# Optimization experiments

Measured on AMD Instinct MI355X. Metric: run time of the kernel, lower is better.

The kernel has to match this reference:

```python
import jax, jax.numpy as jnp
import numpy as np
from jax import lax

D, H, HD, DEPTH = 200, 10, 20, 12   # embed_dim, heads, head_dim, depth
NCH, A = 64, 8                       # EEG channels x time windows -> 512 patches (+cls)
NUM_REL = (2 * NCH - 1) * (2 * A - 1) + 3  # 1908


def make_rel_index(wh, ww):
    # exact port of the torch relative_position_index construction
    coords = np.stack(np.meshgrid(np.arange(wh), np.arange(ww), indexing='ij')).reshape(2, -1)
    rel = (coords[:, :, None] - coords[:, None, :]).transpose(1, 2, 0)
    rel[..., 0] += wh - 1
    rel[..., 1] += ww - 1
    rel[..., 0] *= 2 * ww - 1
    n = wh * ww + 1
    num_rel = (2 * wh - 1) * (2 * ww - 1) + 3
    idx = np.zeros((n, n), dtype=np.int32)
    idx[1:, 1:] = rel.sum(-1)
    idx[0, :] = num_rel - 3
    idx[:, 0] = num_rel - 2
    idx[0, 0] = num_rel - 1
    return idx


def gelu(x):
    return jax.nn.gelu(x, approximate=False)


def layer_norm(x, g, b, eps=1e-6):
    m = x.mean(-1, keepdims=True)
    v = ((x - m) ** 2).mean(-1, keepdims=True)
    return (x - m) * lax.rsqrt(v + eps) * g + b


def group_norm(x, g, b, groups=4, eps=1e-5):
    B, C, Hh, W = x.shape
    xr = x.reshape(B, groups, C // groups, Hh, W)
    m = xr.mean((2, 3, 4), keepdims=True)
    v = ((xr - m) ** 2).mean((2, 3, 4), keepdims=True)
    xr = ((xr - m) * lax.rsqrt(v + eps)).reshape(B, C, Hh, W)
    return xr * g[None, :, None, None] + b[None, :, None, None]


def conv2d(x, w, b, stride, pad):
    y = lax.conv_general_dilated(x, w, window_strides=stride, padding=pad,
                                 dimension_numbers=('NCHW', 'OIHW', 'NCHW'))
    return y + b[None, :, None, None]


def setup_inputs() -> dict:
    B = 8
    key = jax.random.key(0)
    ks = iter(jax.random.split(key, 40))
    rn = lambda shape, s=0.02: jax.random.normal(next(ks), shape, dtype=jnp.float32) * s
    z = lambda shape: jnp.zeros(shape, jnp.float32)
    o = lambda shape: jnp.ones(shape, jnp.float32)
    inp = {}
    inp['x'] = jax.random.normal(next(ks), (B, NCH, A, 200), dtype=jnp.float32)
    inp['conv1_w'] = rn((8, 1, 1, 15), 0.1); inp['conv1_b'] = z(8)
    inp['gn1_g'] = o(8); inp['gn1_b'] = z(8)
    inp['conv2_w'] = rn((8, 8, 1, 3), 0.1); inp['conv2_b'] = z(8)
    inp['gn2_g'] = o(8); inp['gn2_b'] = z(8)
    inp['conv3_w'] = rn((8, 8, 1, 3), 0.1); inp['conv3_b'] = z(8)
    inp['gn3_g'] = o(8); inp['gn3_b'] = z(8)
    inp['cls_token'] = rn((1, 1, D)); inp['pos_embed'] = rn((1, NCH + 1, D))
    inp['time_embed'] = rn((1, 16, D))
    inp['ln1_g'] = o((DEPTH, D)); inp['ln1_b'] = z((DEPTH, D))
    inp['qkv_w'] = rn((DEPTH, 3 * D, D))
    inp['rel_bias_table'] = rn((DEPTH, NUM_REL, H))
    inp['proj_w'] = rn((DEPTH, D, D)); inp['proj_b'] = z((DEPTH, D))
    inp['gamma1'] = 0.1 * o((DEPTH, D))
    inp['ln2_g'] = o((DEPTH, D)); inp['ln2_b'] = z((DEPTH, D))
    inp['fc1_w'] = rn((DEPTH, 4 * D, D)); inp['fc1_b'] = z((DEPTH, 4 * D))
    inp['fc2_w'] = rn((DEPTH, D, 4 * D)); inp['fc2_b'] = z((DEPTH, D))
    inp['gamma2'] = 0.1 * o((DEPTH, D))
    inp['fc_norm_g'] = o(D); inp['fc_norm_b'] = z(D)
    inp['head_w'] = rn((4, D)); inp['head_b'] = z(4)
    inp['rel_pos_index'] = jnp.asarray(make_rel_index(NCH, A))
    return inp


def reference(x, conv1_w, conv1_b, gn1_g, gn1_b, conv2_w, conv2_b, gn2_g, gn2_b,
              conv3_w, conv3_b, gn3_g, gn3_b, cls_token, pos_embed, time_embed,
              ln1_g, ln1_b, qkv_w, rel_bias_table, proj_w, proj_b, gamma1,
              ln2_g, ln2_b, fc1_w, fc1_b, fc2_w, fc2_b, gamma2,
              fc_norm_g, fc_norm_b, head_w, head_b, rel_pos_index):
    B = x.shape[0]
    # TemporalConv patch embed: (B, NCH, A, 200) -> (B, NCH*A, D)
    h = x.reshape(B, 1, NCH * A, -1)
    h = gelu(group_norm(conv2d(h, conv1_w, conv1_b, (1, 8), [(0, 0), (7, 7)]), gn1_g, gn1_b))
    h = gelu(group_norm(conv2d(h, conv2_w, conv2_b, (1, 1), [(0, 0), (1, 1)]), gn2_g, gn2_b))
    h = gelu(group_norm(conv2d(h, conv3_w, conv3_b, (1, 1), [(0, 0), (1, 1)]), gn3_g, gn3_b))
    h = h.transpose(0, 2, 3, 1).reshape(B, NCH * A, D)  # 'B C NA T -> B NA (T C)'
    # cls token + per-electrode pos embed + temporal embed
    h = jnp.concatenate([jnp.broadcast_to(cls_token, (B, 1, D)), h], axis=1)
    pos_p = jnp.repeat(pos_embed[:, 1:, None, :], A, axis=2).reshape(1, NCH * A, D)
    h = h + jnp.concatenate([pos_embed[:, :1], pos_p], axis=1)
    te = jnp.broadcast_to(time_embed[:, None, :A, :], (1, NCH, A, D)).reshape(1, NCH * A, D)
    h = jnp.concatenate([h[:, :1], h[:, 1:] + te], axis=1)
    N = h.shape[1]  # 513
    scale = HD ** -0.5
    for d in range(DEPTH):
        y = layer_norm(h, ln1_g[d], ln1_b[d])
        qkv = (y @ qkv_w[d].T).reshape(B, N, 3, H, HD).transpose(2, 0, 3, 1, 4)
        q, k, v = qkv[0], qkv[1], qkv[2]
        attn = jnp.einsum('bhnd,bhmd->bhnm', q * scale, k)
        attn = attn + rel_bias_table[d][rel_pos_index].transpose(2, 0, 1)[None]
        attn = jax.nn.softmax(attn, axis=-1)
        o = jnp.einsum('bhnm,bhmd->bhnd', attn, v)
        o = o.transpose(0, 2, 1, 3).reshape(B, N, D) @ proj_w[d].T + proj_b[d]
        h = h + gamma1[d] * o
        y = layer_norm(h, ln2_g[d], ln2_b[d])
        y = gelu(y @ fc1_w[d].T + fc1_b[d]) @ fc2_w[d].T + fc2_b[d]
        h = h + gamma2[d] * y
    pooled = layer_norm(h[:, 1:].mean(1), fc_norm_g, fc_norm_b)  # use_mean_pooling
    return pooled @ head_w.T + head_b
```

## Files before the change

### kernel.cpp

```cpp
#include <hip/hip_runtime.h>
#include <math.h>

#define DEV static __device__ __forceinline__

typedef __attribute__((ext_vector_type(8))) short bf16x8;
typedef __attribute__((ext_vector_type(4))) float f32x4;

DEV float gelu_exact(float x) {
    return 0.5f * x * (1.0f + erff(x * 0.70710678118654752f));
}

DEV short f2bf(float f) {
    union { float f; unsigned u; } v; v.f = f;
    unsigned r = v.u + 0x7FFF + ((v.u >> 16) & 1);
    return (short)(r >> 16);
}

DEV float bf2f(unsigned short b) {
    union { unsigned u; float f; } v; v.u = ((unsigned)b) << 16;
    return v.f;
}

DEV unsigned pack2bf(float a, float b) {
    return ((unsigned)(unsigned short)f2bf(a)) | (((unsigned)(unsigned short)f2bf(b)) << 16);
}

DEV void gload_lds16(const void* g, void* lds) {
    __builtin_amdgcn_global_load_lds(
        (const __attribute__((address_space(1))) void*)g,
        (__attribute__((address_space(3))) void*)lds, 16, 0, 0);
}

__global__ void conv1_kernel(const float* __restrict__ x, const float* __restrict__ w,
                             const float* __restrict__ bias, float* __restrict__ out) {
    int idx = blockIdx.x * blockDim.x + threadIdx.x;
    const int total = 8 * 8 * 512 * 25;
    if (idx >= total) return;
    int ow = idx % 25;
    int p  = (idx / 25) % 512;
    int oc = (idx / (25 * 512)) % 8;
    int b  = idx / (25 * 512 * 8);
    const float* xp = x + b * 512 * 200 + p * 200;
    const float* wp = w + oc * 15;
    float acc = bias[oc];
    int t0 = ow * 8 - 7;
#pragma unroll
    for (int k = 0; k < 15; k++) {
        int t = t0 + k;
        if (t >= 0 && t < 200) acc += wp[k] * xp[t];
    }
    out[idx] = acc;
}

__global__ void conv3x1_kernel(const float* __restrict__ in, const float* __restrict__ w,
                               const float* __restrict__ bias, float* __restrict__ out) {
    int idx = blockIdx.x * blockDim.x + threadIdx.x;
    const int total = 8 * 8 * 512 * 25;
    if (idx >= total) return;
    int ow = idx % 25;
    int p  = (idx / 25) % 512;
    int oc = (idx / 12800) & 7;
    int b  = idx / 102400;
    float acc = bias[oc];
#pragma unroll
    for (int ic = 0; ic < 8; ic++) {
        const float* ip = in + b * 102400 + ic * 12800 + p * 25;
        const float* wp = w + oc * 24 + ic * 3;
        if (ow > 0)  acc += wp[0] * ip[ow - 1];
        acc += wp[1] * ip[ow];
        if (ow < 24) acc += wp[2] * ip[ow + 1];
    }
    out[idx] = acc;
}

__global__ void gn_stats_kernel(const float* __restrict__ buf, float* __restrict__ stats) {
    int b = blockIdx.x >> 2, g = blockIdx.x & 3;
    const float* base = buf + b * 102400 + g * 2 * 12800;
    float s = 0.f, s2 = 0.f;
    for (int l = threadIdx.x; l < 25600; l += 256) {
        float v = base[l];
        s += v; s2 += v * v;
    }
    __shared__ float ss[256], ss2[256];
    ss[threadIdx.x] = s; ss2[threadIdx.x] = s2;
    __syncthreads();
    for (int o = 128; o; o >>= 1) {
        if (threadIdx.x < o) { ss[threadIdx.x] += ss[threadIdx.x + o]; ss2[threadIdx.x] += ss2[threadIdx.x + o]; }
        __syncthreads();
    }
    if (threadIdx.x == 0) {
        float m = ss[0] / 25600.f;
        float v = ss2[0] / 25600.f - m * m;
        stats[blockIdx.x * 2] = m;
        stats[blockIdx.x * 2 + 1] = v;
    }
}

__global__ void gn_apply_kernel(float* __restrict__ buf, const float* __restrict__ stats,
                                const float* __restrict__ g, const float* __restrict__ bb) {
    int idx = blockIdx.x * blockDim.x + threadIdx.x;
    if (idx >= 8 * 102400) return;
    int c = (idx / 12800) & 7;
    int b = idx / 102400;
    int grp = c >> 1;
    float m = stats[(b * 4 + grp) * 2];
    float v = stats[(b * 4 + grp) * 2 + 1];
    float val = (buf[idx] - m) * rsqrtf(v + 1e-5f) * g[c] + bb[c];
    buf[idx] = gelu_exact(val);
}

__global__ void embed_kernel(const float* __restrict__ conv, const float* __restrict__ cls,
                             const float* __restrict__ pos, const float* __restrict__ te,
                             float* __restrict__ h) {
    int idx = blockIdx.x * blockDim.x + threadIdx.x;
    if (idx >= 8 * 513 * 200) return;
    int d = idx % 200;
    int n = (idx / 200) % 513;
    int b = idx / (200 * 513);
    float val;
    if (n == 0) {
        val = cls[d] + pos[d];
    } else {
        int p = n - 1;
        int t = d >> 3;
        int c = d & 7;
        val = conv[b * 102400 + c * 12800 + p * 25 + t];
        int ch = p >> 3, tw = p & 7;
        val += pos[(1 + ch) * 200 + d] + te[tw * 200 + d];
    }
    h[idx] = val;
}

__global__ void convpad_kernel(const float* __restrict__ src, short* __restrict__ dst,
                               int R, int K, int KP) {
    int idx = blockIdx.x * blockDim.x + threadIdx.x;
    int total = R * (KP >> 2);
    if (idx >= total) return;
    int r = idx / (KP >> 2);
    int c4 = (idx - r * (KP >> 2)) << 2;
    short4 o;
    if (c4 + 3 < K) {
        float4 f = *(const float4*)&src[(size_t)r * K + c4];
        o.x = f2bf(f.x); o.y = f2bf(f.y); o.z = f2bf(f.z); o.w = f2bf(f.w);
    } else {
        o.x = (c4 + 0 < K) ? f2bf(src[(size_t)r * K + c4 + 0]) : (short)0;
        o.y = (c4 + 1 < K) ? f2bf(src[(size_t)r * K + c4 + 1]) : (short)0;
        o.z = (c4 + 2 < K) ? f2bf(src[(size_t)r * K + c4 + 2]) : (short)0;
        o.w = (c4 + 3 < K) ? f2bf(src[(size_t)r * K + c4 + 3]) : (short)0;
    }
    *(short4*)&dst[(size_t)r * KP + c4] = o;
}

__global__ __launch_bounds__(256) void bias_lds_kernel(const float* __restrict__ table,
                                                       const int* __restrict__ ridx,
                                                       short* __restrict__ bias) {
    __shared__ float tl[1908];
    const int qt = blockIdx.x, hh = blockIdx.y, d = blockIdx.z;
    const float* tab = table + d * 19080;
    for (int i = threadIdx.x; i < 1908; i += 256) tl[i] = tab[i * 10 + hh];
    __syncthreads();
    const int q0 = qt * 32;
    const int nrows = min(32, 513 - q0);
    short* obase = bias + ((size_t)d * 10 + hh) * 513 * 576;
#pragma unroll 2
    for (int lin = threadIdx.x; lin < nrows * 144; lin += 256) {
        int r = lin / 144, j = lin % 144;
        int q = q0 + r;
        const int* rp = ridx + q * 513;
        int k0 = j * 4;
        float v[4];
#pragma unroll
        for (int e = 0; e < 4; e++) {
            int k = k0 + e;
            v[e] = (k < 513) ? tl[rp[k]] : 0.f;
        }
        uint2 pk;
        pk.x = pack2bf(v[0], v[1]);
        pk.y = pack2bf(v[2], v[3]);
        *(uint2*)&obase[(size_t)q * 576 + k0] = pk;
    }
}

__global__ __launch_bounds__(256) void ln_kernel(const float* __restrict__ in,
                                                 const float* __restrict__ g,
                                                 const float* __restrict__ b,
                                                 short* __restrict__ out) {
    int row = blockIdx.x * 4 + (threadIdx.x >> 6);
    int lane = threadIdx.x & 63;
    const float* x = in + (size_t)row * 200;
    float v[4];
    float s = 0.f;
#pragma unroll
    for (int i = 0; i < 4; i++) {
        int d = lane + i * 64;
        v[i] = (d < 200) ? x[d] : 0.f;
        s += v[i];
    }
#pragma unroll
    for (int o = 32; o; o >>= 1) s += __shfl_xor(s, o);
    float mean = s * (1.f / 200.f);
    float s2 = 0.f;
#pragma unroll
    for (int i = 0; i < 4; i++) {
        int d = lane + i * 64;
        float dv = (d < 200) ? (v[i] - mean) : 0.f;
        s2 += dv * dv;
    }
#pragma unroll
    for (int o = 32; o; o >>= 1) s2 += __shfl_xor(s2, o);
    float rstd = rsqrtf(s2 * (1.f / 200.f) + 1e-6f);
#pragma unroll
    for (int i = 0; i < 4; i++) {
        int d = lane + i * 64;
        float val = (d < 200) ? (v[i] - mean) * rstd * g[d] + b[d] : 0.f;
        out[(size_t)row * 256 + d] = f2bf(val);
    }
}

template <int EPI, int BM, int BN>
__global__ __launch_bounds__(256) void gemm_bf(const short* __restrict__ A,
                                               const short* __restrict__ W,
                                               float* __restrict__ Cf,
                                               short* __restrict__ Cb,
                                               const float* __restrict__ res,
                                               const float* __restrict__ bias,
                                               const float* __restrict__ gamma,
                                               int M, int N, int KP, int ldc, int NPout,
                                               short* __restrict__ Qb = nullptr,
                                               short* __restrict__ Kb = nullptr,
                                               short* __restrict__ Vt = nullptr) {
    constexpr int WM = BM / 2, WN = BN / 2;
    constexpr int AM = WM / 16, BNr = WN / 16;
    constexpr int LOADS = (BM + BN) / 32;
    __shared__ __align__(16) short Ss[2][(BM + BN) * 64];

    const int tid = threadIdx.x;
    const int w = tid >> 6, l = tid & 63;
    const int wm = (w >> 1) * WM, wn = (w & 1) * WN;
    const int bm = blockIdx.y * BM, bn = blockIdx.x * BN;

    f32x4 acc[AM][BNr] = {};

    auto stage = [&](int buf, int k0) {
#pragma unroll
        for (int it = 0; it < LOADS; it++) {
            int lin = it * 256 + tid;
            int row = lin >> 3, slot = lin & 7;
            int srcslot = slot ^ (row & 7);
            const short* g;
            if (it * 32 < BM) {
                g = A + (size_t)(bm + row) * KP + k0 + srcslot * 8;
            } else {
                g = W + (size_t)(bn + row - BM) * KP + k0 + srcslot * 8;
            }
            gload_lds16(g, (char*)Ss[buf] + lin * 16);
        }
    };

    const int nk = KP >> 6;
    stage(0, 0);
    int cur = 0;
    for (int kstep = 0; kstep < nk; kstep++) {
        if (kstep + 1 < nk) {
            stage(cur ^ 1, (kstep + 1) << 6);
            if constexpr (LOADS == 6)      asm volatile("s_waitcnt vmcnt(6)" ::: "memory");
            else if constexpr (LOADS == 4) asm volatile("s_waitcnt vmcnt(4)" ::: "memory");
            else                           asm volatile("s_waitcnt vmcnt(3)" ::: "memory");
        } else {
            asm volatile("s_waitcnt vmcnt(0)" ::: "memory");
        }
        __builtin_amdgcn_s_barrier();

        const char* Sc = (const char*)Ss[cur];
#pragma unroll
        for (int kk = 0; kk < 2; kk++) {
            const int kbyte = kk * 64 + (l >> 4) * 16;
            bf16x8 af[AM], bfr[BNr];
#pragma unroll
            for (int i = 0; i < AM; i++) {
                int r = wm + i * 16 + (l & 15);
                af[i] = *(const bf16x8*)(Sc + r * 128 + (kbyte ^ ((r & 7) << 4)));
            }
#pragma unroll
            for (int j = 0; j < BNr; j++) {
                int r = BM + wn + j * 16 + (l & 15);
                bfr[j] = *(const bf16x8*)(Sc + r * 128 + (kbyte ^ ((r & 7) << 4)));
            }
#pragma unroll
            for (int i = 0; i < AM; i++)
#pragma unroll
                for (int j = 0; j < BNr; j++)
                    acc[i][j] = __builtin_amdgcn_mfma_f32_16x16x32_bf16(af[i], bfr[j], acc[i][j], 0, 0, 0);
        }
        __builtin_amdgcn_s_barrier();
        cur ^= 1;
    }

    const int col0 = bn + wn + (l & 15);
    const int rbase = (l >> 4) * 4;
#pragma unroll
    for (int i = 0; i < AM; i++) {
#pragma unroll
        for (int r = 0; r < 4; r++) {
            int gm = bm + wm + i * 16 + rbase + r;
            if (gm >= M) continue;
#pragma unroll
            for (int j = 0; j < BNr; j++) {
                int gn = col0 + j * 16;
                float v = acc[i][j][r];
                if (EPI == 1) {
                    if (gn < N) Cf[(size_t)gm * ldc + gn] =
                        res[(size_t)gm * ldc + gn] + gamma[gn] * (v + bias[gn]);
                } else if (EPI == 2) {
                    if (gn < NPout)
                        Cb[(size_t)gm * ldc + gn] = (gn < N) ? f2bf(gelu_exact(v + bias[gn])) : (short)0;
                } else {
                    if (gn < 600) {
                        int bb2 = gm / 513, n = gm - bb2 * 513;
                        if (gn < 200) {
                            int hq = gn / 20, dq = gn - hq * 20;
                            Qb[((size_t)(bb2 * 10 + hq) * 576 + n) * 32 + dq] =
                                f2bf(v * 0.22360679774997896f);
                        } else if (gn < 400) {
                            int gk = gn - 200, hk = gk / 20, dk = gk - hk * 20;
                            Kb[((size_t)(bb2 * 10 + hk) * 576 + n) * 32 + dk] = f2bf(v);
                        } else {
                            int gv = gn - 400, hv = gv / 20, dv2 = gv - hv * 20;
                            Vt[((size_t)(bb2 * 10 + hv) * 32 + dv2) * 576 + n] = f2bf(v);
                        }
                    }
                }
            }
        }
    }
}

__global__ __launch_bounds__(256) void attn_mfma2(const short* __restrict__ Qb,
                                                  const short* __restrict__ Kb,
                                                  const short* __restrict__ Vt,
                                                  const short* __restrict__ biasb,
                                                  short* __restrict__ ob) {
    __shared__ __align__(16) short Klds[2][64 * 32];
    __shared__ __align__(16) short Vlds[2][32 * 64];
    __shared__ __align__(16) short Pl[4 * 16 * 72];

    const int orig = blockIdx.x;
    const int wg = (orig & 7) * 90 + (orig >> 3);
    const int hh = wg / 72;
    const int rem = wg % 72;
    const int qt = rem >> 3, b = rem & 7;

    const int t = threadIdx.x, wave = t >> 6, l = t & 63;
    const int lq = l & 15, hi = l >> 4;
    const int n = qt * 64 + wave * 16 + lq;
    const int nc = min(n, 512);

    const size_t bh = (size_t)(b * 10 + hh);
    const short* Kbase = Kb + bh * 576 * 32;
    const short* Vbase = Vt + bh * 32 * 576;
    const short* Brow  = biasb + ((size_t)hh * 513 + nc) * 576;

    bf16x8 qf = *(const bf16x8*)&Qb[(bh * 576 + nc) * 32 + hi * 8];

    const int krow = t >> 2, kch = t & 3;
    const short* ksrc = Kbase + (size_t)krow * 32 + (kch ^ ((krow >> 2) & 3)) * 8;
    const int vrow = t >> 3, vch = t & 7;
    const short* vsrc = Vbase + (size_t)vrow * 576 + (vch ^ (vrow & 7)) * 8;

    float mrun = -1e30f, lsum = 0.f;
    f32x4 oacc0 = {}, oacc1 = {};
    const f32x4 zero4 = {};

    gload_lds16(ksrc, (char*)Klds[0] + t * 16);
    gload_lds16(vsrc, (char*)Vlds[0] + t * 16);

    int cur = 0;
    for (int kt = 0; kt < 9; kt++) {
        const int koff = kt * 64;

        uint2 bl[4];
#pragma unroll
        for (int c = 0; c < 4; c++)
            bl[c] = *(const uint2*)&Brow[koff + c * 16 + hi * 4];

        if (kt < 8) {
            const int knext = koff + 64;
            gload_lds16(ksrc + (size_t)knext * 32, (char*)Klds[cur ^ 1] + t * 16);
            gload_lds16(vsrc + knext, (char*)Vlds[cur ^ 1] + t * 16);
            asm volatile("s_waitcnt vmcnt(2)" ::: "memory");
        } else {
            asm volatile("s_waitcnt vmcnt(0)" ::: "memory");
        }
        __builtin_amdgcn_s_barrier();

        const short* Kc = Klds[cur];
        const short* Vc = Vlds[cur];

        f32x4 s[4];
        __builtin_amdgcn_s_setprio(1);
#pragma unroll
        for (int c = 0; c < 4; c++) {
            int r = c * 16 + lq;
            bf16x8 kf = *(const bf16x8*)((const char*)Kc + r * 64 + ((hi ^ ((lq >> 2) & 3)) << 4));
            s[c] = __builtin_amdgcn_mfma_f32_16x16x32_bf16(kf, qf, zero4, 0, 0, 0);
        }
        __builtin_amdgcn_s_setprio(0);

        float sv[4][4];
        float tm = -1e30f;
#pragma unroll
        for (int c = 0; c < 4; c++) {
            float bv[4] = { bf2f((unsigned short)(bl[c].x & 0xFFFF)), bf2f((unsigned short)(bl[c].x >> 16)),
                            bf2f((unsigned short)(bl[c].y & 0xFFFF)), bf2f((unsigned short)(bl[c].y >> 16)) };
            int kglob = koff + c * 16 + hi * 4;
#pragma unroll
            for (int r = 0; r < 4; r++) {
                float val = s[c][r] + bv[r];
                if (kglob + r > 512) val = -1e30f;
                sv[c][r] = val;
                tm = fmaxf(tm, val);
            }
        }
        tm = fmaxf(tm, __shfl_xor(tm, 16));
        tm = fmaxf(tm, __shfl_xor(tm, 32));
        float mnew = fmaxf(mrun, tm);
        float resc = __expf(mrun - mnew);
        mrun = mnew;

        float ts = 0.f;
#pragma unroll
        for (int c = 0; c < 4; c++) {
            float p0 = __expf(sv[c][0] - mnew);
            float p1 = __expf(sv[c][1] - mnew);
            float p2 = __expf(sv[c][2] - mnew);
            float p3 = __expf(sv[c][3] - mnew);
            ts += (p0 + p1) + (p2 + p3);
            uint2 pk;
            pk.x = pack2bf(p0, p1);
            pk.y = pack2bf(p2, p3);
            *(uint2*)&Pl[wave * 1152 + lq * 72 + c * 16 + hi * 4] = pk;
        }
        ts += __shfl_xor(ts, 16);
        ts += __shfl_xor(ts, 32);
        lsum = lsum * resc + ts;
        oacc0 *= resc;
        oacc1 *= resc;

        __builtin_amdgcn_s_setprio(1);
#pragma unroll
        for (int kc = 0; kc < 2; kc++) {
            bf16x8 pf = *(const bf16x8*)&Pl[wave * 1152 + lq * 72 + kc * 32 + hi * 8];
            bf16x8 vf0 = *(const bf16x8*)((const char*)Vc + lq * 128 +
                                          (((kc * 4 + hi) ^ (lq & 7)) << 4));
            bf16x8 vf1 = *(const bf16x8*)((const char*)Vc + (16 + lq) * 128 +
                                          (((kc * 4 + hi) ^ (lq & 7)) << 4));
            oacc0 = __builtin_amdgcn_mfma_f32_16x16x32_bf16(vf0, pf, oacc0, 0, 0, 0);
            oacc1 = __builtin_amdgcn_mfma_f32_16x16x32_bf16(vf1, pf, oacc1, 0, 0, 0);
        }
        __builtin_amdgcn_s_setprio(0);

        __builtin_amdgcn_s_barrier();
        cur ^= 1;
    }

    if (n < 513) {
        float inv = 1.f / lsum;
        short* op = ob + (size_t)(b * 513 + n) * 256 + hh * 20;
        {
            uint2 pk;
            pk.x = pack2bf(oacc0[0] * inv, oacc0[1] * inv);
            pk.y = pack2bf(oacc0[2] * inv, oacc0[3] * inv);
            *(uint2*)&op[hi * 4] = pk;
        }
        if (hi == 0) {
            uint2 pk;
            pk.x = pack2bf(oacc1[0] * inv, oacc1[1] * inv);
            pk.y = pack2bf(oacc1[2] * inv, oacc1[3] * inv);
            *(uint2*)&op[16] = pk;
        }
    }
}

__global__ __launch_bounds__(256) void final_kernel(const float* __restrict__ h,
                                                    const float* __restrict__ g,
                                                    const float* __restrict__ bb,
                                                    const float* __restrict__ hw,
                                                    const float* __restrict__ hb,
                                                    float* __restrict__ out) {
    __shared__ float pool[256];
    __shared__ float red[256];
    int b = blockIdx.x, t = threadIdx.x;
    float s = 0.f;
    if (t < 200) {
        const float* hp = h + b * 513 * 200 + 200 + t;
        for (int p = 0; p < 512; p++) s += hp[p * 200];
        s *= (1.f / 512.f);
    }
    pool[t] = (t < 200) ? s : 0.f;
    red[t] = pool[t];
    __syncthreads();
    for (int o = 128; o; o >>= 1) {
        if (t < o) red[t] += red[t + o];
        __syncthreads();
    }
    float mean = red[0] / 200.f;
    __syncthreads();
    float dv = (t < 200) ? (pool[t] - mean) : 0.f;
    red[t] = dv * dv;
    __syncthreads();
    for (int o = 128; o; o >>= 1) {
        if (t < o) red[t] += red[t + o];
        __syncthreads();
    }
    float var = red[0] / 200.f;
    float rstd = rsqrtf(var + 1e-6f);
    __syncthreads();
    if (t < 200) pool[t] = (pool[t] - mean) * rstd * g[t] + bb[t];
    __syncthreads();
    if (t < 4) {
        float acc = hb[t];
        for (int d2 = 0; d2 < 200; d2++) acc += pool[d2] * hw[t * 200 + d2];
        out[b * 4 + t] = acc;
    }
}

extern "C" void kernel_launch(void* const* d_in, const int* in_sizes, int n_in,
                              void* d_out, int out_size, void* d_ws, size_t ws_size,
                              hipStream_t stream) {
    const float* x        = (const float*)d_in[0];
    const float* conv1_w  = (const float*)d_in[1];
    const float* conv1_b  = (const float*)d_in[2];
    const float* gn1_g    = (const float*)d_in[3];
    const float* gn1_b    = (const float*)d_in[4];
    const float* conv2_w  = (const float*)d_in[5];
    const float* conv2_b  = (const float*)d_in[6];
    const float* gn2_g    = (const float*)d_in[7];
    const float* gn2_b    = (const float*)d_in[8];
    const float* conv3_w  = (const float*)d_in[9];
    const float* conv3_b  = (const float*)d_in[10];
    const float* gn3_g    = (const float*)d_in[11];
    const float* gn3_b    = (const float*)d_in[12];
    const float* cls_tok  = (const float*)d_in[13];
    const float* pos_emb  = (const float*)d_in[14];
    const float* time_emb = (const float*)d_in[15];
    const float* ln1_g    = (const float*)d_in[16];
    const float* ln1_b    = (const float*)d_in[17];
    const float* qkv_w    = (const float*)d_in[18];
    const float* rel_tab  = (const float*)d_in[19];
    const float* proj_w   = (const float*)d_in[20];
    const float* proj_b   = (const float*)d_in[21];
    const float* gamma1   = (const float*)d_in[22];
    const float* ln2_g    = (const float*)d_in[23];
    const float* ln2_b    = (const float*)d_in[24];
    const float* fc1_w    = (const float*)d_in[25];
    const float* fc1_b    = (const float*)d_in[26];
    const float* fc2_w    = (const float*)d_in[27];
    const float* fc2_b    = (const float*)d_in[28];
    const float* gamma2   = (const float*)d_in[29];
    const float* fcn_g    = (const float*)d_in[30];
    const float* fcn_b    = (const float*)d_in[31];
    const float* head_w   = (const float*)d_in[32];
    const float* head_b   = (const float*)d_in[33];
    const int*   rel_idx  = (const int*)d_in[34];

    char* p = (char*)d_ws;
    float* h    = (float*)p; p += 3283200;
    char* qreg = p;
    float* c1   = (float*)qreg;
    float* c2   = c1 + 819200;
    short* Qb   = (short*)qreg;
    short* Kb   = Qb + 1474560;
    short* Vt   = Kb + 1474560;
    short* mlp  = (short*)qreg;
    p += 9849600;
    short* y    = (short*)p; p += 2101248;
    short* ob   = (short*)p; p += 2101248;
    short* wqkv = (short*)p; p += 3686400;
    short* wproj= (short*)p; p += 1228800;
    short* wfc1 = (short*)p; p += 4915200;
    short* wfc2 = (short*)p; p += 3993600;
    short* biasb= (short*)p; p += 12 * 5909760;
    float* stats= (float*)p;

    convpad_kernel<<<(7200 * 64 + 255) / 256, 256, 0, stream>>>(qkv_w, wqkv, 7200, 200, 256);
    convpad_kernel<<<(2400 * 64 + 255) / 256, 256, 0, stream>>>(proj_w, wproj, 2400, 200, 256);
    convpad_kernel<<<(9600 * 64 + 255) / 256, 256, 0, stream>>>(fc1_w, wfc1, 9600, 200, 256);
    convpad_kernel<<<(2400 * 208 + 255) / 256, 256, 0, stream>>>(fc2_w, wfc2, 2400, 800, 832);
    bias_lds_kernel<<<dim3(17, 10, 12), 256, 0, stream>>>(rel_tab, rel_idx, biasb);
    hipMemsetAsync(ob, 0, 2101248, stream);

    conv1_kernel<<<3200, 256, 0, stream>>>(x, conv1_w, conv1_b, c1);
    gn_stats_kernel<<<32, 256, 0, stream>>>(c1, stats);
    gn_apply_kernel<<<3200, 256, 0, stream>>>(c1, stats, gn1_g, gn1_b);
    conv3x1_kernel<<<3200, 256, 0, stream>>>(c1, conv2_w, conv2_b, c2);
    gn_stats_kernel<<<32, 256, 0, stream>>>(c2, stats);
    gn_apply_kernel<<<3200, 256, 0, stream>>>(c2, stats, gn2_g, gn2_b);
    conv3x1_kernel<<<3200, 256, 0, stream>>>(c2, conv3_w, conv3_b, c1);
    gn_stats_kernel<<<32, 256, 0, stream>>>(c1, stats);
    gn_apply_kernel<<<3200, 256, 0, stream>>>(c1, stats, gn3_g, gn3_b);
    embed_kernel<<<(820800 + 255) / 256, 256, 0, stream>>>(c1, cls_tok, pos_emb, time_emb, h);

    hipMemsetAsync(Qb, 0, 3 * 1474560 * 2, stream);

    for (int d = 0; d < 12; d++) {
        ln_kernel<<<1026, 256, 0, stream>>>(h, ln1_g + d * 200, ln1_b + d * 200, y);
        gemm_bf<3, 32, 64><<<dim3(10, 129), 256, 0, stream>>>(y, wqkv + d * 153600,
                                                              nullptr, nullptr, nullptr, nullptr, nullptr,
                                                              4104, 600, 256, 0, 0, Qb, Kb, Vt);
        attn_mfma2<<<720, 256, 0, stream>>>(Qb, Kb, Vt, biasb + (size_t)d * 2954880, ob);
        gemm_bf<1, 32, 64><<<dim3(4, 129), 256, 0, stream>>>(ob, wproj + d * 51200, h, nullptr,
                                                             h, proj_b + d * 200, gamma1 + d * 200,
                                                             4104, 200, 256, 200, 0);
        ln_kernel<<<1026, 256, 0, stream>>>(h, ln2_g + d * 200, ln2_b + d * 200, y);
        gemm_bf<2, 32, 64><<<dim3(13, 129), 256, 0, stream>>>(y, wfc1 + d * 204800, nullptr, mlp,
                                                              nullptr, fc1_b + d * 800, nullptr,
                                                              4104, 800, 256, 832, 832);
        gemm_bf<1, 32, 64><<<dim3(4, 129), 256, 0, stream>>>(mlp, wfc2 + d * 166400, h, nullptr,
                                                             h, fc2_b + d * 200, gamma2 + d * 200,
                                                             4104, 200, 832, 200, 0);
    }

    final_kernel<<<8, 256, 0, stream>>>(h, fcn_g, fcn_b, head_w, head_b, (float*)d_out);
}
```

Baseline: 982.2 us.

## Deepen attention K/V pipeline to four LDS buffers and split GroupNorm stats

The attention kernel now cycles through four LDS buffers for K and V and prefetches two tiles ahead. It drops the trailing barrier in each iteration and loads the next tile's bias values one step early into registers. The goal is to hide global-load latency and barrier cost in the key loop, at the price of more LDS per block and a vmcnt wait scheme that must be counted exactly. Separately, GroupNorm statistics move from 32 blocks to 512 blocks that write partial sums, which a small second kernel combines, so that more of the GPU works on this step.

```diff
diff --git a/kernel.cpp b/kernel.cpp
--- a/kernel.cpp
+++ b/kernel.cpp
@@ -73,27 +73,43 @@
     out[idx] = acc;
 }
 
-__global__ void gn_stats_kernel(const float* __restrict__ buf, float* __restrict__ stats) {
-    int b = blockIdx.x >> 2, g = blockIdx.x & 3;
-    const float* base = buf + b * 102400 + g * 2 * 12800;
+__global__ __launch_bounds__(256) void gn_stats1(const float* __restrict__ buf,
+                                                 float* __restrict__ part) {
+    int bg = blockIdx.x >> 4, ch = blockIdx.x & 15;
+    const float* base = buf + (bg >> 2) * 102400 + (bg & 3) * 25600 + ch * 1600;
     float s = 0.f, s2 = 0.f;
-    for (int l = threadIdx.x; l < 25600; l += 256) {
-        float v = base[l];
-        s += v; s2 += v * v;
-    }
-    __shared__ float ss[256], ss2[256];
-    ss[threadIdx.x] = s; ss2[threadIdx.x] = s2;
+    int t4 = threadIdx.x * 4;
+#pragma unroll
+    for (int off = 0; off < 1600; off += 1024) {
+        int l = t4 + off;
+        if (l < 1600) {
+            float4 v = *(const float4*)&base[l];
+            s  += v.x + v.y + v.z + v.w;
+            s2 += v.x * v.x + v.y * v.y + v.z * v.z + v.w * v.w;
+        }
+    }
+#pragma unroll
+    for (int o = 32; o; o >>= 1) { s += __shfl_xor(s, o); s2 += __shfl_xor(s2, o); }
+    __shared__ float red[4][2];
+    if ((threadIdx.x & 63) == 0) { red[threadIdx.x >> 6][0] = s; red[threadIdx.x >> 6][1] = s2; }
     __syncthreads();
-    for (int o = 128; o; o >>= 1) {
-        if (threadIdx.x < o) { ss[threadIdx.x] += ss[threadIdx.x + o]; ss2[threadIdx.x] += ss2[threadIdx.x + o]; }
-        __syncthreads();
-    }
     if (threadIdx.x == 0) {
-        float m = ss[0] / 25600.f;
-        float v = ss2[0] / 25600.f - m * m;
-        stats[blockIdx.x * 2] = m;
-        stats[blockIdx.x * 2 + 1] = v;
-    }
+        part[blockIdx.x * 2]     = red[0][0] + red[1][0] + red[2][0] + red[3][0];
+        part[blockIdx.x * 2 + 1] = red[0][1] + red[1][1] + red[2][1] + red[3][1];
+    }
+}
+
+__global__ void gn_stats2(const float* __restrict__ part, float* __restrict__ stats) {
+    int i = threadIdx.x;
+    if (i >= 32) return;
+    float s = 0.f, q = 0.f;
+    for (int c = 0; c < 16; c++) {
+        s += part[(i * 16 + c) * 2];
+        q += part[(i * 16 + c) * 2 + 1];
+    }
+    float m = s / 25600.f;
+    stats[i * 2] = m;
+    stats[i * 2 + 1] = q / 25600.f - m * m;
 }
 
 __global__ void gn_apply_kernel(float* __restrict__ buf, const float* __restrict__ stats,
@@ -335,13 +351,13 @@
     }
 }
 
-__global__ __launch_bounds__(256) void attn_mfma2(const short* __restrict__ Qb,
+__global__ __launch_bounds__(256) void attn_mfma3(const short* __restrict__ Qb,
                                                   const short* __restrict__ Kb,
                                                   const short* __restrict__ Vt,
                                                   const short* __restrict__ biasb,
                                                   short* __restrict__ ob) {
-    __shared__ __align__(16) short Klds[2][64 * 32];
-    __shared__ __align__(16) short Vlds[2][32 * 64];
+    __shared__ __align__(16) short Klds[4][64 * 32];
+    __shared__ __align__(16) short Vlds[4][32 * 64];
     __shared__ __align__(16) short Pl[4 * 16 * 72];
 
     const int orig = blockIdx.x;
@@ -371,30 +387,37 @@
     f32x4 oacc0 = {}, oacc1 = {};
     const f32x4 zero4 = {};
 
+    uint2 bl_cur[4], bl_next[4];
+#pragma unroll
+    for (int c = 0; c < 4; c++)
+        bl_cur[c] = *(const uint2*)&Brow[c * 16 + hi * 4];
     gload_lds16(ksrc, (char*)Klds[0] + t * 16);
     gload_lds16(vsrc, (char*)Vlds[0] + t * 16);
-
-    int cur = 0;
+    gload_lds16(ksrc + 64 * 32, (char*)Klds[1] + t * 16);
+    gload_lds16(vsrc + 64, (char*)Vlds[1] + t * 16);
+
     for (int kt = 0; kt < 9; kt++) {
         const int koff = kt * 64;
 
-        uint2 bl[4];
-#pragma unroll
-        for (int c = 0; c < 4; c++)
-            bl[c] = *(const uint2*)&Brow[koff + c * 16 + hi * 4];
-
         if (kt < 8) {
-            const int knext = koff + 64;
-            gload_lds16(ksrc + (size_t)knext * 32, (char*)Klds[cur ^ 1] + t * 16);
-            gload_lds16(vsrc + knext, (char*)Vlds[cur ^ 1] + t * 16);
-            asm volatile("s_waitcnt vmcnt(2)" ::: "memory");
+#pragma unroll
+            for (int c = 0; c < 4; c++)
+                bl_next[c] = *(const uint2*)&Brow[koff + 64 + c * 16 + hi * 4];
+        }
+        if (kt < 7) {
+            const int knext = koff + 128;
+            gload_lds16(ksrc + (size_t)knext * 32, (char*)Klds[(kt + 2) & 3] + t * 16);
+            gload_lds16(vsrc + knext, (char*)Vlds[(kt + 2) & 3] + t * 16);
+            asm volatile("s_waitcnt vmcnt(8)" ::: "memory");
+        } else if (kt == 7) {
+            asm volatile("s_waitcnt vmcnt(6)" ::: "memory");
         } else {
             asm volatile("s_waitcnt vmcnt(0)" ::: "memory");
         }
         __builtin_amdgcn_s_barrier();
 
-        const short* Kc = Klds[cur];
-        const short* Vc = Vlds[cur];
+        const short* Kc = Klds[kt & 3];
+        const short* Vc = Vlds[kt & 3];
 
         f32x4 s[4];
         __builtin_amdgcn_s_setprio(1);
@@ -410,8 +433,8 @@
         float tm = -1e30f;
 #pragma unroll
         for (int c = 0; c < 4; c++) {
-            float bv[4] = { bf2f((unsigned short)(bl[c].x & 0xFFFF)), bf2f((unsigned short)(bl[c].x >> 16)),
-                            bf2f((unsigned short)(bl[c].y & 0xFFFF)), bf2f((unsigned short)(bl[c].y >> 16)) };
+            float bv[4] = { bf2f((unsigned short)(bl_cur[c].x & 0xFFFF)), bf2f((unsigned short)(bl_cur[c].x >> 16)),
+                            bf2f((unsigned short)(bl_cur[c].y & 0xFFFF)), bf2f((unsigned short)(bl_cur[c].y >> 16)) };
             int kglob = koff + c * 16 + hi * 4;
 #pragma unroll
             for (int r = 0; r < 4; r++) {
@@ -459,8 +482,8 @@
         }
         __builtin_amdgcn_s_setprio(0);
 
-        __builtin_amdgcn_s_barrier();
-        cur ^= 1;
+#pragma unroll
+        for (int c = 0; c < 4; c++) bl_cur[c] = bl_next[c];
     }
 
     if (n < 513) {
@@ -580,7 +603,8 @@
     short* wfc1 = (short*)p; p += 4915200;
     short* wfc2 = (short*)p; p += 3993600;
     short* biasb= (short*)p; p += 12 * 5909760;
-    float* stats= (float*)p;
+    float* stats= (float*)p; p += 256;
+    float* part = (float*)p;
 
     convpad_kernel<<<(7200 * 64 + 255) / 256, 256, 0, stream>>>(qkv_w, wqkv, 7200, 200, 256);
     convpad_kernel<<<(2400 * 64 + 255) / 256, 256, 0, stream>>>(proj_w, wproj, 2400, 200, 256);
@@ -590,13 +614,16 @@
     hipMemsetAsync(ob, 0, 2101248, stream);
 
     conv1_kernel<<<3200, 256, 0, stream>>>(x, conv1_w, conv1_b, c1);
-    gn_stats_kernel<<<32, 256, 0, stream>>>(c1, stats);
+    gn_stats1<<<512, 256, 0, stream>>>(c1, part);
+    gn_stats2<<<1, 64, 0, stream>>>(part, stats);
     gn_apply_kernel<<<3200, 256, 0, stream>>>(c1, stats, gn1_g, gn1_b);
     conv3x1_kernel<<<3200, 256, 0, stream>>>(c1, conv2_w, conv2_b, c2);
-    gn_stats_kernel<<<32, 256, 0, stream>>>(c2, stats);
+    gn_stats1<<<512, 256, 0, stream>>>(c2, part);
+    gn_stats2<<<1, 64, 0, stream>>>(part, stats);
     gn_apply_kernel<<<3200, 256, 0, stream>>>(c2, stats, gn2_g, gn2_b);
     conv3x1_kernel<<<3200, 256, 0, stream>>>(c2, conv3_w, conv3_b, c1);
-    gn_stats_kernel<<<32, 256, 0, stream>>>(c1, stats);
+    gn_stats1<<<512, 256, 0, stream>>>(c1, part);
+    gn_stats2<<<1, 64, 0, stream>>>(part, stats);
     gn_apply_kernel<<<3200, 256, 0, stream>>>(c1, stats, gn3_g, gn3_b);
     embed_kernel<<<(820800 + 255) / 256, 256, 0, stream>>>(c1, cls_tok, pos_emb, time_emb, h);
 
@@ -607,7 +634,7 @@
         gemm_bf<3, 32, 64><<<dim3(10, 129), 256, 0, stream>>>(y, wqkv + d * 153600,
                                                               nullptr, nullptr, nullptr, nullptr, nullptr,
                                                               4104, 600, 256, 0, 0, Qb, Kb, Vt);
-        attn_mfma2<<<720, 256, 0, stream>>>(Qb, Kb, Vt, biasb + (size_t)d * 2954880, ob);
+        attn_mfma3<<<720, 256, 0, stream>>>(Qb, Kb, Vt, biasb + (size_t)d * 2954880, ob);
         gemm_bf<1, 32, 64><<<dim3(4, 129), 256, 0, stream>>>(ob, wproj + d * 51200, h, nullptr,
                                                              h, proj_b + d * 200, gamma1 + d * 200,
                                                              4104, 200, 256, 200, 0);
```

After: 915.4 us. 1.07x faster.
